# Optimization experiments

Hardware: AMD Instinct MI355X
Metric: run time of the kernel (lower is better)

Reference implementation:

```python
import jax, jax.numpy as jnp
import numpy as np

B, N, IN_DIM, SLOT_DIM, HIDDEN = 32, 4096, 256, 256, 512
NUM_SLOTS, NUM_ITERS = 8, 3
EPS_LN = 1e-5


def layernorm(x, g, b):
    m = jnp.mean(x, axis=-1, keepdims=True)
    v = jnp.var(x, axis=-1, keepdims=True)
    return (x - m) * jax.lax.rsqrt(v + EPS_LN) * g + b


def setup_inputs() -> dict:
    key = jax.random.key(0)
    ks = jax.random.split(key, 16)
    s = 0.02
    return {
        "inputs": jax.random.normal(ks[0], (B, N, IN_DIM), jnp.float32),
        "init_noise": jax.random.normal(ks[1], (B, NUM_SLOTS, SLOT_DIM), jnp.float32),
        "mu": jax.random.normal(ks[2], (1, 1, SLOT_DIM), jnp.float32),
        "sigma_raw": jax.random.normal(ks[3], (1, 1, SLOT_DIM), jnp.float32),
        "ln_in_g": jnp.ones((IN_DIM,), jnp.float32), "ln_in_b": jnp.zeros((IN_DIM,), jnp.float32),
        "ln_s_g": jnp.ones((SLOT_DIM,), jnp.float32), "ln_s_b": jnp.zeros((SLOT_DIM,), jnp.float32),
        "ln_m_g": jnp.ones((SLOT_DIM,), jnp.float32), "ln_m_b": jnp.zeros((SLOT_DIM,), jnp.float32),
        "wq": jax.random.normal(ks[4], (SLOT_DIM, SLOT_DIM), jnp.float32) * s,
        "bq": jnp.zeros((SLOT_DIM,), jnp.float32),
        "wk": jax.random.normal(ks[5], (SLOT_DIM, IN_DIM), jnp.float32) * s,
        "bk": jnp.zeros((SLOT_DIM,), jnp.float32),
        "wv": jax.random.normal(ks[6], (SLOT_DIM, IN_DIM), jnp.float32) * s,
        "bv": jnp.zeros((SLOT_DIM,), jnp.float32),
        "w_ih": jax.random.normal(ks[7], (3 * SLOT_DIM, SLOT_DIM), jnp.float32) * s,
        "w_hh": jax.random.normal(ks[8], (3 * SLOT_DIM, SLOT_DIM), jnp.float32) * s,
        "b_ih": jnp.zeros((3 * SLOT_DIM,), jnp.float32),
        "b_hh": jnp.zeros((3 * SLOT_DIM,), jnp.float32),
        "w1": jax.random.normal(ks[9], (HIDDEN, SLOT_DIM), jnp.float32) * s,
        "b1": jnp.zeros((HIDDEN,), jnp.float32),
        "w2": jax.random.normal(ks[10], (SLOT_DIM, HIDDEN), jnp.float32) * s,
        "b2": jnp.zeros((SLOT_DIM,), jnp.float32),
    }


def gru_cell(x, h, w_ih, w_hh, b_ih, b_hh):
    # PyTorch GRUCell: gates split as (reset, update, new)
    gx = x @ w_ih.T + b_ih
    gh = h @ w_hh.T + b_hh
    xr, xz, xn = jnp.split(gx, 3, axis=-1)
    hr, hz, hn = jnp.split(gh, 3, axis=-1)
    r = jax.nn.sigmoid(xr + hr)
    z = jax.nn.sigmoid(xz + hz)
    n = jnp.tanh(xn + r * hn)
    return (1.0 - z) * n + z * h


def reference(inputs, init_noise, mu, sigma_raw, ln_in_g, ln_in_b, ln_s_g, ln_s_b,
              ln_m_g, ln_m_b, wq, bq, wk, bk, wv, bv, w_ih, w_hh, b_ih, b_hh,
              w1, b1, w2, b2):
    scale = SLOT_DIM ** (-0.5)
    x = layernorm(inputs, ln_in_g, ln_in_b)          # [B,N,Din]
    k = x @ wk.T + bk                                # [B,N,D]
    v = x @ wv.T + bv                                # [B,N,D]
    sigma = jax.nn.softplus(sigma_raw)
    slots = mu + sigma * init_noise                  # [B,S,D]
    attn = None
    for _ in range(NUM_ITERS):
        slots_prev = slots
        q = layernorm(slots, ln_s_g, ln_s_b) @ wq.T + bq      # [B,S,D]
        logits = jnp.einsum('bnd,bsd->bns', k, q) * scale     # [B,N,S]
        attn = jax.nn.softmax(logits, axis=-1) + 1e-8         # softmax over slots
        attn = attn / jnp.sum(attn, axis=1, keepdims=True)    # renorm over inputs
        updates = jnp.einsum('bnd,bns->bsd', v, attn)         # [B,S,D]
        slots = gru_cell(updates, slots_prev, w_ih, w_hh, b_ih, b_hh)
        h = jax.nn.relu(layernorm(slots, ln_m_g, ln_m_b) @ w1.T + b1)
        slots = slots + (h @ w2.T + b2)
    return slots, attn
```

## Files before the change

### kernel.cpp

```cpp
#include <hip/hip_runtime.h>
#include <hip/hip_fp16.h>
#include <cstdint>

#define DEV static __device__ __forceinline__

typedef _Float16 f16x2 __attribute__((ext_vector_type(2)));
typedef _Float16 f16x8 __attribute__((ext_vector_type(8)));
typedef float    f32x4 __attribute__((ext_vector_type(4)));

DEV float fdot2u(uint32_t a, uint32_t b, float c){
  union U { uint32_t u; f16x2 h; };
  U ua; ua.u = a; U ub; ub.u = b;
#if __has_builtin(__builtin_amdgcn_fdot2)
  return __builtin_amdgcn_fdot2(ua.h, ub.h, c, false);
#else
  return c + (float)ua.h[0]*(float)ub.h[0] + (float)ua.h[1]*(float)ub.h[1];
#endif
}

DEV float dot4(uint4 x, uint4 w, float a){
  a = fdot2u(x.x, w.x, a); a = fdot2u(x.y, w.y, a);
  a = fdot2u(x.z, w.z, a); a = fdot2u(x.w, w.w, a);
  return a;
}

DEV float wsum64(float v){
  #pragma unroll
  for (int o = 32; o; o >>= 1) v += __shfl_xor(v, o);
  return v;
}

DEV uint32_t pack2h(float a, float b){
  __half ha = __float2half(a), hb = __float2half(b);
  return (uint32_t)__half_as_ushort(ha) | ((uint32_t)__half_as_ushort(hb) << 16);
}

DEV uint32_t packsh(float v){
  float o = __shfl_xor(v, 1);
  return pack2h(v, o);
}

DEV uint4 packrow8(const float* p){
  uint4 r;
  r.x = pack2h(p[0], p[1]); r.y = pack2h(p[2], p[3]);
  r.z = pack2h(p[4], p[5]); r.w = pack2h(p[6], p[7]);
  return r;
}

DEV void gld16(const void* g, void* l){
  __builtin_amdgcn_global_load_lds(
      (const __attribute__((address_space(1))) void*)g,
      (__attribute__((address_space(3))) void*)l, 16, 0, 0);
}

__global__ __launch_bounds__(256) void k_lntr(
  const float* __restrict__ xin, const float* __restrict__ lng,
  const float* __restrict__ lnb, uint32_t* __restrict__ xhat,
  const float* __restrict__ wq, const float* __restrict__ wv,
  const float* __restrict__ wih, const float* __restrict__ whh,
  const float* __restrict__ w1, const float* __restrict__ w2,
  const float* __restrict__ wk,
  uint4* __restrict__ WQp4, uint4* __restrict__ WVp4,
  uint4* __restrict__ WIHp4, uint4* __restrict__ WHHp4,
  uint4* __restrict__ W1p4, uint4* __restrict__ W2p4,
  uint4* __restrict__ WKp4)
{
  if (blockIdx.x >= 32768){
    int u = (blockIdx.x - 32768) * 256 + threadIdx.x;
    if (u < 8192){
      int e4 = u >> 8, n = u & 255;
      WVp4[u] = packrow8(wv + n*256 + 8*e4);
    } else if (u < 32768){
      int v = u - 8192; int e4 = v / 768, n = v - e4*768;
      WIHp4[v] = packrow8(wih + n*256 + 8*e4);
    } else if (u < 57344){
      int v = u - 32768; int e4 = v / 768, n = v - e4*768;
      WHHp4[v] = packrow8(whh + n*256 + 8*e4);
    } else if (u < 73728){
      int v = u - 57344; int e4 = v >> 9, n = v & 511;
      W1p4[v] = packrow8(w1 + n*256 + 8*e4);
    } else if (u < 90112){
      int v = u - 73728; int e4 = v >> 8, n = v & 255;
      W2p4[v] = packrow8(w2 + n*512 + 8*e4);
    } else if (u < 98304){
      int v = u - 90112; int e4 = v >> 8, n = v & 255;
      WQp4[v] = packrow8(wq + n*256 + 8*e4);
    } else if (u < 106496){
      int v = u - 98304; int d4 = v >> 8, c = v & 255;
      uint4 r;
      r.x = pack2h(wk[(8*d4+0)*256 + c], wk[(8*d4+1)*256 + c]);
      r.y = pack2h(wk[(8*d4+2)*256 + c], wk[(8*d4+3)*256 + c]);
      r.z = pack2h(wk[(8*d4+4)*256 + c], wk[(8*d4+5)*256 + c]);
      r.w = pack2h(wk[(8*d4+6)*256 + c], wk[(8*d4+7)*256 + c]);
      WKp4[v] = r;
    }
    return;
  }
  int row = blockIdx.x * 4 + (threadIdx.x >> 6);
  int lane = threadIdx.x & 63;
  const float4 xv = ((const float4*)(xin + (size_t)row * 256))[lane];
  float s1 = wsum64(xv.x + xv.y + xv.z + xv.w);
  float s2 = wsum64(xv.x*xv.x + xv.y*xv.y + xv.z*xv.z + xv.w*xv.w);
  float m = s1 * (1.0f/256.0f);
  float var = s2 * (1.0f/256.0f) - m*m;
  float rstd = rsqrtf(var + 1e-5f);
  float4 gv = ((const float4*)lng)[lane];
  float4 bv = ((const float4*)lnb)[lane];
  float y0 = (xv.x - m)*rstd*gv.x + bv.x;
  float y1 = (xv.y - m)*rstd*gv.y + bv.y;
  float y2 = (xv.z - m)*rstd*gv.z + bv.z;
  float y3 = (xv.w - m)*rstd*gv.w + bv.w;
  ((uint2*)(xhat + (size_t)row * 128))[lane] = make_uint2(pack2h(y0,y1), pack2h(y2,y3));
}

template<int MODE>
__global__ __launch_bounds__(512) void k_slot(
  const float* __restrict__ noise, const float* __restrict__ mu,
  const float* __restrict__ sigraw,
  const float* S0, float* SDST,
  const float* __restrict__ UAp, const float* __restrict__ ASp,
  float* __restrict__ AS,
  const uint4* __restrict__ WVp4, const float* __restrict__ bv,
  const uint4* __restrict__ WIHp4, const uint4* __restrict__ WHHp4,
  const float* __restrict__ bih, const float* __restrict__ bhh,
  const float* __restrict__ lmg, const float* __restrict__ lmb,
  const uint4* __restrict__ W1p4, const float* __restrict__ b1,
  const uint4* __restrict__ W2p4, const float* __restrict__ b2,
  const float* __restrict__ lsg, const float* __restrict__ lsb,
  const uint4* __restrict__ WQp4, const float* __restrict__ bq,
  const uint4* __restrict__ WKp4, const float* __restrict__ bk,
  uint32_t* __restrict__ QTH, float* __restrict__ CV)
{
  __shared__ float gx[768], gh[768];
  __shared__ float part[512];
  __shared__ uint4 hs4[32], un4[32], us4[32], sln4[32], q4[32];
  __shared__ uint4 hb4[64];
  __shared__ float redA[8], redB[8];

  const int t = threadIdx.x;
  const int h = t >> 8;
  const int c = t & 255;
  const int lane = t & 63;
  const int w8 = t >> 6;
  const int r = blockIdx.x;
  const int b = r >> 3, s = r & 7;

  float snv = 0.f, spv = 0.f;

  if (MODE == 0){
    if (t < 256){
      float x = sigraw[c];
      float sp = (x > 20.0f) ? x : log1pf(__expf(x));
      snv = mu[c] + sp * noise[r*256 + c];
      SDST[r*256 + c] = snv;
    }
  } else {
    if (w8 == 0){
      float v = (lane < 16) ? ASp[lane*256 + r] : 0.f;
      v += __shfl_xor(v, 1); v += __shfl_xor(v, 2);
      v += __shfl_xor(v, 4); v += __shfl_xor(v, 8);
      if (lane == 0) redA[0] = v;
    }
    __syncthreads();
    const float asum_r = redA[0];
    if (MODE == 2 && t == 0) AS[r] = asum_r;
    const float ainv = 1.0f / asum_r;
    float hv = 0.f;
    if (t < 256){
      hv = S0[r*256 + c];
      float us = 0.f;
      #pragma unroll
      for (int ch = 0; ch < 16; ++ch) us += UAp[ch*65536 + r*256 + c];
      float unv = us * ainv;
      uint32_t ph = packsh(hv), pu = packsh(unv);
      if (!(c & 1)){
        ((uint32_t*)hs4)[c>>1] = ph;
        ((uint32_t*)un4)[c>>1] = pu;
      }
    }
    __syncthreads();

    {
      float a = 0.f;
      #pragma unroll 8
      for (int e4 = h*16; e4 < h*16 + 16; ++e4)
        a = dot4(un4[e4], WVp4[e4*256 + c], a);
      part[t] = a;
    }
    __syncthreads();
    if (t < 256){
      float us = part[t] + part[t + 256] + bv[c];
      uint32_t p = packsh(us);
      if (!(c & 1)) ((uint32_t*)us4)[c>>1] = p;
    }
    __syncthreads();

    {
      const uint4* IN4 = h ? hs4 : us4;
      const uint4* WP = h ? WHHp4 : WIHp4;
      float a0 = 0.f, a1 = 0.f, a2 = 0.f;
      #pragma unroll 8
      for (int e4 = 0; e4 < 32; ++e4){
        uint4 x = IN4[e4];
        a0 = dot4(x, WP[e4*768 + c], a0);
        a1 = dot4(x, WP[e4*768 + 256 + c], a1);
        a2 = dot4(x, WP[e4*768 + 512 + c], a2);
      }
      float* OUT = h ? gh : gx;
      OUT[c] = a0; OUT[256 + c] = a1; OUT[512 + c] = a2;
    }
    __syncthreads();

    if (t < 256){
      float xr = gx[c]     + bih[c];
      float xz = gx[256+c] + bih[256+c];
      float xn = gx[512+c] + bih[512+c];
      float hr = gh[c]     + bhh[c];
      float hz = gh[256+c] + bhh[256+c];
      float hn = gh[512+c] + bhh[512+c];
      float rg = 1.f/(1.f + __expf(-(xr + hr)));
      float zg = 1.f/(1.f + __expf(-(xz + hz)));
      float ng = tanhf(xn + rg*hn);
      spv = (1.f - zg)*ng + zg*hv;
      float a = wsum64(spv), bs = wsum64(spv*spv);
      if (lane == 0){ redA[w8] = a; redB[w8] = bs; }
    }
    __syncthreads();
    {
      float s1 = redA[0]+redA[1]+redA[2]+redA[3];
      float s2 = redB[0]+redB[1]+redB[2]+redB[3];
      float m = s1*(1.f/256.f), var = s2*(1.f/256.f) - m*m;
      float rstd = rsqrtf(var + 1e-5f);
      if (t < 256){
        float slv = (spv - m)*rstd*lmg[c] + lmb[c];
        uint32_t p = packsh(slv);
        if (!(c & 1)) ((uint32_t*)sln4)[c>>1] = p;
      }
    }
    __syncthreads();

    {
      float a = 0.f;
      #pragma unroll 8
      for (int e4 = 0; e4 < 32; ++e4)
        a = dot4(sln4[e4], W1p4[e4*512 + t], a);
      float hval = fmaxf(a + b1[t], 0.f);
      float o = __shfl_xor(hval, 1);
      if (!(t & 1)) ((uint32_t*)hb4)[t>>1] = pack2h(hval, o);
    }
    __syncthreads();

    {
      float a = 0.f;
      #pragma unroll 8
      for (int e4 = h*32; e4 < h*32 + 32; ++e4)
        a = dot4(hb4[e4], W2p4[e4*256 + c], a);
      part[t] = a;
    }
    __syncthreads();
    if (t < 256){
      snv = spv + part[t] + part[t + 256] + b2[c];
      SDST[r*256 + c] = snv;
    }
  }

  if (MODE != 2){
    if (t < 256){
      float a = wsum64(snv), bs = wsum64(snv*snv);
      if (lane == 0){ redA[w8] = a; redB[w8] = bs; }
    }
    __syncthreads();
    {
      float s1 = redA[0]+redA[1]+redA[2]+redA[3];
      float s2 = redB[0]+redB[1]+redB[2]+redB[3];
      float m = s1*(1.f/256.f), var = s2*(1.f/256.f) - m*m;
      float rstd = rsqrtf(var + 1e-5f);
      if (t < 256){
        float slv = (snv - m)*rstd*lsg[c] + lsb[c];
        uint32_t p = packsh(slv);
        if (!(c & 1)) ((uint32_t*)sln4)[c>>1] = p;
      }
    }
    __syncthreads();

    {
      float a = 0.f;
      #pragma unroll 8
      for (int e4 = h*16; e4 < h*16 + 16; ++e4)
        a = dot4(sln4[e4], WQp4[e4*256 + c], a);
      part[t] = a;
    }
    __syncthreads();
    if (t < 256){
      float qv = part[t] + part[t + 256] + bq[c];
      float p = wsum64(bk[c] * qv);
      if (lane == 0) redA[w8] = p;
      uint32_t pk = packsh(qv);
      if (!(c & 1)) ((uint32_t*)q4)[c>>1] = pk;
    }
    __syncthreads();
    {
      float cv = redA[0]+redA[1]+redA[2]+redA[3];
      if (t == 0) CV[r] = cv;
    }

    {
      float a = 0.f;
      #pragma unroll 8
      for (int e4 = h*16; e4 < h*16 + 16; ++e4)
        a = dot4(q4[e4], WKp4[e4*256 + c], a);
      part[t] = a;
    }
    __syncthreads();
    if (t < 256){
      float qtv = part[t] + part[t + 256];
      uint32_t p = packsh(qtv);
      if (!(c & 1)) QTH[b*1024 + (c>>1)*8 + s] = p;
    }
  }
}

template<bool LAST>
__global__ __launch_bounds__(256) void k_attn(
  const uint32_t* __restrict__ xhat,
  const uint32_t* __restrict__ qtpk, const float* __restrict__ cvec,
  float* __restrict__ UAp, float* __restrict__ ASp,
  float* __restrict__ attn_out)
{
  __shared__ uint32_t xs[8192];
  __shared__ uint32_t qs[1024];
  __shared__ float attn_lds[64][16];
  __shared__ float up_lds[8][256];
  __shared__ float as_red[4][8];

  const int b = blockIdx.y, chunk = blockIdx.x;
  const int t = threadIdx.x;
  const int l = t & 63, w = t >> 6;
  const int g = l >> 4, sl = l & 15;

  const size_t base = (size_t)b*4096 + (size_t)chunk*256;

  for (int i = t; i < 1024; i += 256) qs[i] = qtpk[b*1024 + i];

  auto stage = [&](int st){
    const size_t gr0 = base + (size_t)st*64;
    #pragma unroll
    for (int i = 0; i < 8; ++i){
      int n  = w*8 + i;
      int rl = 2*n + (l >> 5);
      int ql = (l & 31) ^ (rl & 7);
      gld16(xhat + (gr0 + rl)*128 + ql*4, xs + n*256);
    }
  };

  stage(0);
  __syncthreads();

  uint4 bq[8];
  #pragma unroll
  for (int kk = 0; kk < 8; ++kk){
    if (sl < 8){
      uint4 v;
      v.x = qs[(16*kk + 4*g + 0)*8 + sl];
      v.y = qs[(16*kk + 4*g + 1)*8 + sl];
      v.z = qs[(16*kk + 4*g + 2)*8 + sl];
      v.w = qs[(16*kk + 4*g + 3)*8 + sl];
      bq[kk] = v;
    } else bq[kk] = make_uint4(0u,0u,0u,0u);
  }
  const float cv = (sl < 8) ? cvec[b*8 + sl] : 0.f;

  float up[8][4];
  #pragma unroll
  for (int s = 0; s < 8; ++s){ up[s][0]=0.f; up[s][1]=0.f; up[s][2]=0.f; up[s][3]=0.f; }
  float asl_acc = 0.f;

  for (int st = 0; st < 4; ++st){
    if (st){ __syncthreads(); stage(st); __syncthreads(); }
    const int L0 = 16*w;

    f32x4 acc; acc[0]=0.f; acc[1]=0.f; acc[2]=0.f; acc[3]=0.f;
    const int rowA = L0 + sl;
    #pragma unroll
    for (int kk = 0; kk < 8; ++kk){
      uint4 av = *(const uint4*)(xs + rowA*128 + (((4*kk + g) ^ (rowA & 7)) << 2));
      union { uint4 u; f16x8 h; } A, B;
      A.u = av; B.u = bq[kk];
      acc = __builtin_amdgcn_mfma_f32_16x16x32_f16(A.h, B.h, acc, 0, 0, 0);
    }

    #pragma unroll
    for (int reg = 0; reg < 4; ++reg){
      float d = (acc[reg] + cv) * 0.0625f;
      float m = d;
      m = fmaxf(m, __shfl_xor(m, 1));
      m = fmaxf(m, __shfl_xor(m, 2));
      m = fmaxf(m, __shfl_xor(m, 4));
      float e = __expf(d - m);
      float ssum = e;
      ssum += __shfl_xor(ssum, 1);
      ssum += __shfl_xor(ssum, 2);
      ssum += __shfl_xor(ssum, 4);
      float a = e / ssum + 1e-8f;
      asl_acc += a;
      attn_lds[L0 + 4*g + reg][sl] = a;
    }

    #pragma unroll 4
    for (int rr = 0; rr < 16; ++rr){
      const int row = L0 + rr;
      const uint32_t* xp = xs + row*128 + ((((l>>1) ^ (row & 7)) << 2) | ((l & 1) << 1));
      uint2 xv = *(const uint2*)xp;
      float x0 = __half2float(__ushort_as_half((unsigned short)(xv.x & 0xffff)));
      float x1 = __half2float(__ushort_as_half((unsigned short)(xv.x >> 16)));
      float x2 = __half2float(__ushort_as_half((unsigned short)(xv.y & 0xffff)));
      float x3 = __half2float(__ushort_as_half((unsigned short)(xv.y >> 16)));
      const float4 a0 = *(const float4*)&attn_lds[row][0];
      const float4 a1 = *(const float4*)&attn_lds[row][4];
      float as8[8] = {a0.x, a0.y, a0.z, a0.w, a1.x, a1.y, a1.z, a1.w};
      #pragma unroll
      for (int s = 0; s < 8; ++s){
        up[s][0] += as8[s]*x0; up[s][1] += as8[s]*x1;
        up[s][2] += as8[s]*x2; up[s][3] += as8[s]*x3;
      }
    }

    if (LAST){
      __syncthreads();
      int row = t >> 2, s0 = (t & 3)*2;
      float2 v = *(const float2*)&attn_lds[row][s0];
      *(float2*)(attn_out + (base + (size_t)st*64 + row)*8 + s0) = v;
    }
  }

  {
    float v = asl_acc;
    v += __shfl_xor(v, 16);
    v += __shfl_xor(v, 32);
    if (l < 8) as_red[w][l] = v;
  }

  __syncthreads();
  #pragma unroll
  for (int ww = 0; ww < 4; ++ww){
    if (w == ww){
      #pragma unroll
      for (int s = 0; s < 8; ++s){
        float4* dst = (float4*)&up_lds[s][l*4];
        float4 v = make_float4(up[s][0], up[s][1], up[s][2], up[s][3]);
        if (ww){ float4 o = *dst; v.x += o.x; v.y += o.y; v.z += o.z; v.w += o.w; }
        *dst = v;
      }
    }
    __syncthreads();
  }
  #pragma unroll
  for (int s = 0; s < 8; ++s)
    UAp[(size_t)chunk*65536 + (size_t)(b*8 + s)*256 + t] = up_lds[s][t];
  if (t < 8)
    ASp[chunk*256 + b*8 + t] = as_red[0][t] + as_red[1][t] + as_red[2][t] + as_red[3][t];
}

__global__ __launch_bounds__(256) void k_out(
  const float* __restrict__ AS, float* __restrict__ out)
{
  int j = blockIdx.x * 256 + threadIdx.x;
  int b = j >> 15;
  int s = j & 7;
  out[65536 + j] = out[65536 + j] * (1.0f / AS[b*8 + s]);
}

extern "C" void kernel_launch(void* const* d_in, const int* in_sizes, int n_in,
                              void* d_out, int out_size, void* d_ws, size_t ws_size,
                              hipStream_t stream) {
  const float* inputs = (const float*)d_in[0];
  const float* noise  = (const float*)d_in[1];
  const float* mu     = (const float*)d_in[2];
  const float* sigraw = (const float*)d_in[3];
  const float* lng    = (const float*)d_in[4];
  const float* lnb    = (const float*)d_in[5];
  const float* lsg    = (const float*)d_in[6];
  const float* lsb    = (const float*)d_in[7];
  const float* lmg    = (const float*)d_in[8];
  const float* lmb    = (const float*)d_in[9];
  const float* wq     = (const float*)d_in[10];
  const float* bq     = (const float*)d_in[11];
  const float* wk     = (const float*)d_in[12];
  const float* bk     = (const float*)d_in[13];
  const float* wv     = (const float*)d_in[14];
  const float* bv     = (const float*)d_in[15];
  const float* wih    = (const float*)d_in[16];
  const float* whh    = (const float*)d_in[17];
  const float* bih    = (const float*)d_in[18];
  const float* bhh    = (const float*)d_in[19];
  const float* w1     = (const float*)d_in[20];
  const float* b1     = (const float*)d_in[21];
  const float* w2     = (const float*)d_in[22];
  const float* b2     = (const float*)d_in[23];
  float* out = (float*)d_out;

  char* w = (char*)d_ws;
  size_t o = 0;
  uint32_t* XH = (uint32_t*)w;  o += 67108864;
  uint32_t* QT = (uint32_t*)(w + o); o += 131072;
  float* CV  = (float*)(w + o); o += 1024;
  float* AS  = (float*)(w + o); o += 1024;
  float* S0  = (float*)(w + o); o += 262144;
  uint4* WQp = (uint4*)(w + o); o += 131072;
  uint4* WVp = (uint4*)(w + o); o += 131072;
  uint4* WIHp= (uint4*)(w + o); o += 393216;
  uint4* WHHp= (uint4*)(w + o); o += 393216;
  uint4* W1p = (uint4*)(w + o); o += 262144;
  uint4* W2p = (uint4*)(w + o); o += 262144;
  uint4* WKp = (uint4*)(w + o); o += 131072;
  float* UAp = (float*)(w + o); o += 4194304;
  float* ASp = (float*)(w + o); o += 16384;

  k_lntr<<<33184, 256, 0, stream>>>(inputs, lng, lnb, XH,
                                    wq, wv, wih, whh, w1, w2, wk,
                                    WQp, WVp, WIHp, WHHp, W1p, W2p, WKp);
  k_slot<0><<<256, 512, 0, stream>>>(noise, mu, sigraw, S0, S0, UAp, ASp, AS,
      WVp, bv, WIHp, WHHp, bih, bhh, lmg, lmb, W1p, b1, W2p, b2,
      lsg, lsb, WQp, bq, WKp, bk, QT, CV);

  dim3 ga(16, 32);
  for (int it = 0; it < 3; ++it){
    if (it == 2) k_attn<true ><<<ga, 256, 0, stream>>>(XH, QT, CV, UAp, ASp, out + 65536);
    else         k_attn<false><<<ga, 256, 0, stream>>>(XH, QT, CV, UAp, ASp, out + 65536);
    if (it < 2)
      k_slot<1><<<256, 512, 0, stream>>>(noise, mu, sigraw, S0, S0, UAp, ASp, AS,
          WVp, bv, WIHp, WHHp, bih, bhh, lmg, lmb, W1p, b1, W2p, b2,
          lsg, lsb, WQp, bq, WKp, bk, QT, CV);
    else
      k_slot<2><<<256, 512, 0, stream>>>(noise, mu, sigraw, S0, out, UAp, ASp, AS,
          WVp, bv, WIHp, WHHp, bih, bhh, lmg, lmb, W1p, b1, W2p, b2,
          lsg, lsb, WQp, bq, WKp, bk, QT, CV);
  }
  k_out<<<4096, 256, 0, stream>>>(AS, out);
}
```

Measured before the change: 373.6 us.

## Double-buffer attention LDS staging and fuse attn renormalization into final slot kernel

Measured after the change: 377.3 us. Within noise of the previous version (+1.0%).

```diff
diff --git a/kernel.cpp b/kernel.cpp
--- a/kernel.cpp
+++ b/kernel.cpp
@@ -119,7 +119,7 @@
   const float* __restrict__ sigraw,
   const float* S0, float* SDST,
   const float* __restrict__ UAp, const float* __restrict__ ASp,
-  float* __restrict__ AS,
+  float* __restrict__ OUTA,
   const uint4* __restrict__ WVp4, const float* __restrict__ bv,
   const uint4* __restrict__ WIHp4, const uint4* __restrict__ WHHp4,
   const float* __restrict__ bih, const float* __restrict__ bhh,
@@ -136,6 +136,7 @@
   __shared__ uint4 hs4[32], un4[32], us4[32], sln4[32], q4[32];
   __shared__ uint4 hb4[64];
   __shared__ float redA[8], redB[8];
+  __shared__ float asb[8];
 
   const int t = threadIdx.x;
   const int h = t >> 8;
@@ -155,15 +156,23 @@
       SDST[r*256 + c] = snv;
     }
   } else {
-    if (w8 == 0){
-      float v = (lane < 16) ? ASp[lane*256 + r] : 0.f;
-      v += __shfl_xor(v, 1); v += __shfl_xor(v, 2);
-      v += __shfl_xor(v, 4); v += __shfl_xor(v, 8);
-      if (lane == 0) redA[0] = v;
-    }
-    __syncthreads();
-    const float asum_r = redA[0];
-    if (MODE == 2 && t == 0) AS[r] = asum_r;
+    if (MODE == 2){
+      if (lane < 16){
+        float v = ASp[lane*256 + b*8 + w8];
+        v += __shfl_xor(v, 1); v += __shfl_xor(v, 2);
+        v += __shfl_xor(v, 4); v += __shfl_xor(v, 8);
+        if (lane == 0) asb[w8] = v;
+      }
+    } else {
+      if (w8 == 0){
+        float v = (lane < 16) ? ASp[lane*256 + r] : 0.f;
+        v += __shfl_xor(v, 1); v += __shfl_xor(v, 2);
+        v += __shfl_xor(v, 4); v += __shfl_xor(v, 8);
+        if (lane == 0) redA[0] = v;
+      }
+    }
+    __syncthreads();
+    const float asum_r = (MODE == 2) ? asb[s] : redA[0];
     const float ainv = 1.0f / asum_r;
     float hv = 0.f;
     if (t < 256){
@@ -317,6 +326,18 @@
       uint32_t p = packsh(qtv);
       if (!(c & 1)) QTH[b*1024 + (c>>1)*8 + s] = p;
     }
+  } else if (s == 0){
+    float inv[8];
+    #pragma unroll
+    for (int j = 0; j < 8; ++j) inv[j] = 1.0f / asb[j];
+    float4* ap = (float4*)(OUTA + (size_t)b * 32768);
+    #pragma unroll 4
+    for (int i = t; i < 8192; i += 512){
+      float4 v = ap[i];
+      int h4 = (i & 1) * 4;
+      v.x *= inv[h4+0]; v.y *= inv[h4+1]; v.z *= inv[h4+2]; v.w *= inv[h4+3];
+      ap[i] = v;
+    }
   }
 }
 
@@ -327,11 +348,11 @@
   float* __restrict__ UAp, float* __restrict__ ASp,
   float* __restrict__ attn_out)
 {
-  __shared__ uint32_t xs[8192];
+  __shared__ __align__(16) uint32_t xs[2][8192];
   __shared__ uint32_t qs[1024];
   __shared__ float attn_lds[64][16];
-  __shared__ float up_lds[8][256];
   __shared__ float as_red[4][8];
+  float* up_lds = (float*)&xs[0][0];
 
   const int b = blockIdx.y, chunk = blockIdx.x;
   const int t = threadIdx.x;
@@ -343,13 +364,14 @@
   for (int i = t; i < 1024; i += 256) qs[i] = qtpk[b*1024 + i];
 
   auto stage = [&](int st){
+    uint32_t* dst = &xs[st & 1][0];
     const size_t gr0 = base + (size_t)st*64;
     #pragma unroll
     for (int i = 0; i < 8; ++i){
       int n  = w*8 + i;
       int rl = 2*n + (l >> 5);
       int ql = (l & 31) ^ (rl & 7);
-      gld16(xhat + (gr0 + rl)*128 + ql*4, xs + n*256);
+      gld16(xhat + (gr0 + rl)*128 + ql*4, dst + n*256);
     }
   };
 
@@ -376,14 +398,16 @@
   float asl_acc = 0.f;
 
   for (int st = 0; st < 4; ++st){
-    if (st){ __syncthreads(); stage(st); __syncthreads(); }
+    if (st) __syncthreads();
+    if (st < 3) stage(st + 1);
+    const uint32_t* xb = &xs[st & 1][0];
     const int L0 = 16*w;
 
     f32x4 acc; acc[0]=0.f; acc[1]=0.f; acc[2]=0.f; acc[3]=0.f;
     const int rowA = L0 + sl;
     #pragma unroll
     for (int kk = 0; kk < 8; ++kk){
-      uint4 av = *(const uint4*)(xs + rowA*128 + (((4*kk + g) ^ (rowA & 7)) << 2));
+      uint4 av = *(const uint4*)(xb + rowA*128 + (((4*kk + g) ^ (rowA & 7)) << 2));
       union { uint4 u; f16x8 h; } A, B;
       A.u = av; B.u = bq[kk];
       acc = __builtin_amdgcn_mfma_f32_16x16x32_f16(A.h, B.h, acc, 0, 0, 0);
@@ -409,7 +433,7 @@
     #pragma unroll 4
     for (int rr = 0; rr < 16; ++rr){
       const int row = L0 + rr;
-      const uint32_t* xp = xs + row*128 + ((((l>>1) ^ (row & 7)) << 2) | ((l & 1) << 1));
+      const uint32_t* xp = xb + row*128 + ((((l>>1) ^ (row & 7)) << 2) | ((l & 1) << 1));
       uint2 xv = *(const uint2*)xp;
       float x0 = __half2float(__ushort_as_half((unsigned short)(xv.x & 0xffff)));
       float x1 = __half2float(__ushort_as_half((unsigned short)(xv.x >> 16)));
@@ -446,7 +470,7 @@
     if (w == ww){
       #pragma unroll
       for (int s = 0; s < 8; ++s){
-        float4* dst = (float4*)&up_lds[s][l*4];
+        float4* dst = (float4*)&up_lds[s*256 + l*4];
         float4 v = make_float4(up[s][0], up[s][1], up[s][2], up[s][3]);
         if (ww){ float4 o = *dst; v.x += o.x; v.y += o.y; v.z += o.z; v.w += o.w; }
         *dst = v;
@@ -456,18 +480,9 @@
   }
   #pragma unroll
   for (int s = 0; s < 8; ++s)
-    UAp[(size_t)chunk*65536 + (size_t)(b*8 + s)*256 + t] = up_lds[s][t];
+    UAp[(size_t)chunk*65536 + (size_t)(b*8 + s)*256 + t] = up_lds[s*256 + t];
   if (t < 8)
     ASp[chunk*256 + b*8 + t] = as_red[0][t] + as_red[1][t] + as_red[2][t] + as_red[3][t];
-}
-
-__global__ __launch_bounds__(256) void k_out(
-  const float* __restrict__ AS, float* __restrict__ out)
-{
-  int j = blockIdx.x * 256 + threadIdx.x;
-  int b = j >> 15;
-  int s = j & 7;
-  out[65536 + j] = out[65536 + j] * (1.0f / AS[b*8 + s]);
 }
 
 extern "C" void kernel_launch(void* const* d_in, const int* in_sizes, int n_in,
@@ -504,7 +519,6 @@
   uint32_t* XH = (uint32_t*)w;  o += 67108864;
   uint32_t* QT = (uint32_t*)(w + o); o += 131072;
   float* CV  = (float*)(w + o); o += 1024;
-  float* AS  = (float*)(w + o); o += 1024;
   float* S0  = (float*)(w + o); o += 262144;
   uint4* WQp = (uint4*)(w + o); o += 131072;
   uint4* WVp = (uint4*)(w + o); o += 131072;
@@ -516,25 +530,26 @@
   float* UAp = (float*)(w + o); o += 4194304;
   float* ASp = (float*)(w + o); o += 16384;
 
+  float* OUTA = out + 65536;
+
   k_lntr<<<33184, 256, 0, stream>>>(inputs, lng, lnb, XH,
                                     wq, wv, wih, whh, w1, w2, wk,
                                     WQp, WVp, WIHp, WHHp, W1p, W2p, WKp);
-  k_slot<0><<<256, 512, 0, stream>>>(noise, mu, sigraw, S0, S0, UAp, ASp, AS,
+  k_slot<0><<<256, 512, 0, stream>>>(noise, mu, sigraw, S0, S0, UAp, ASp, OUTA,
       WVp, bv, WIHp, WHHp, bih, bhh, lmg, lmb, W1p, b1, W2p, b2,
       lsg, lsb, WQp, bq, WKp, bk, QT, CV);
 
   dim3 ga(16, 32);
   for (int it = 0; it < 3; ++it){
-    if (it == 2) k_attn<true ><<<ga, 256, 0, stream>>>(XH, QT, CV, UAp, ASp, out + 65536);
-    else         k_attn<false><<<ga, 256, 0, stream>>>(XH, QT, CV, UAp, ASp, out + 65536);
+    if (it == 2) k_attn<true ><<<ga, 256, 0, stream>>>(XH, QT, CV, UAp, ASp, OUTA);
+    else         k_attn<false><<<ga, 256, 0, stream>>>(XH, QT, CV, UAp, ASp, OUTA);
     if (it < 2)
-      k_slot<1><<<256, 512, 0, stream>>>(noise, mu, sigraw, S0, S0, UAp, ASp, AS,
+      k_slot<1><<<256, 512, 0, stream>>>(noise, mu, sigraw, S0, S0, UAp, ASp, OUTA,
           WVp, bv, WIHp, WHHp, bih, bhh, lmg, lmb, W1p, b1, W2p, b2,
           lsg, lsb, WQp, bq, WKp, bk, QT, CV);
     else
-      k_slot<2><<<256, 512, 0, stream>>>(noise, mu, sigraw, S0, out, UAp, ASp, AS,
+      k_slot<2><<<256, 512, 0, stream>>>(noise, mu, sigraw, S0, out, UAp, ASp, OUTA,
           WVp, bv, WIHp, WHHp, bih, bhh, lmg, lmb, W1p, b1, W2p, b2,
           lsg, lsb, WQp, bq, WKp, bk, QT, CV);
   }
-  k_out<<<4096, 256, 0, stream>>>(AS, out);
-}
+}
```
